# Kernel tuning notes

Hardware: AMD Instinct MI355X
Metric: run time of the kernel (lower is better)

The kernel has to match this reference:

```python
import jax, jax.numpy as jnp
import numpy as np


def setup_inputs() -> dict:
    key = jax.random.key(0)
    ks = jax.random.split(key, 7)
    SEQ, B, IN, H, OUT = 1024, 1024, 57, 128, 18
    return {
        "line_tensor": jax.random.normal(ks[0], (SEQ, B, IN), dtype=jnp.float32),
        "W_ih": jax.random.normal(ks[1], (H, IN), dtype=jnp.float32) * 0.1,
        "b_ih": jax.random.normal(ks[2], (H,), dtype=jnp.float32) * 0.1,
        "W_hh": jax.random.normal(ks[3], (H, H), dtype=jnp.float32) * 0.1,
        "b_hh": jax.random.normal(ks[4], (H,), dtype=jnp.float32) * 0.1,
        "W_ho": jax.random.normal(ks[5], (OUT, H), dtype=jnp.float32) * 0.1,
        "b_ho": jax.random.normal(ks[6], (OUT,), dtype=jnp.float32) * 0.1,
    }


def reference(line_tensor, W_ih, b_ih, W_hh, b_hh, W_ho, b_ho):
    # Elman RNN: h_t = tanh(i2h(x_t) + h2h(h_{t-1})); output = log_softmax(h2o(h_T))
    B = line_tensor.shape[1]
    H = W_hh.shape[0]
    h0 = jnp.zeros((B, H), dtype=line_tensor.dtype)

    def step(h, x):  # x: [B, IN], h: [B, H]
        h = jnp.tanh(x @ W_ih.T + b_ih + h @ W_hh.T + b_hh)
        return h, None

    hT, _ = jax.lax.scan(step, h0, line_tensor)
    logits = hT @ W_ho.T + b_ho  # [B, OUT]
    out = jax.nn.log_softmax(logits, axis=1)
    return (out, hT)
```

## Files before the change

kernel.cpp:

```cpp
#include <hip/hip_runtime.h>
#include <math.h>

#define SEQ   1024
#define BATCH 1024
#define IN_F  57
#define H_F   128
#define OUT_F 18
#define MROWS 16
#define HSTR  136
#define XSTR  72

typedef __attribute__((ext_vector_type(8))) short bf8;
typedef __attribute__((ext_vector_type(4))) float f32x4;

static __device__ __forceinline__ short f2bf(float f) {
    unsigned u = __builtin_bit_cast(unsigned, f);
    u = (u + 0x7FFFu + ((u >> 16) & 1u)) >> 16;
    return (short)u;
}
static __device__ __forceinline__ float bf2f(short s) {
    unsigned u = ((unsigned)(unsigned short)s) << 16;
    return __builtin_bit_cast(float, u);
}

__global__ __launch_bounds__(256) void rnn_mfma_kernel(
    const float* __restrict__ X,
    const float* __restrict__ W_ih,
    const float* __restrict__ b_ih,
    const float* __restrict__ W_hh,
    const float* __restrict__ b_hh,
    const float* __restrict__ W_ho,
    const float* __restrict__ b_ho,
    float* __restrict__ out)
{
    const int tid  = threadIdx.x;
    const int lane = tid & 63;
    const int wv   = tid >> 6;
    const int n16  = lane & 15;
    const int quad = lane >> 4;
    const int b0   = blockIdx.x * MROWS;

    __shared__ short h_lds[2][MROWS][HSTR];
    __shared__ short x_lds[2][MROWS][XSTR];
    __shared__ float logits_lds[MROWS][OUT_F];
    __shared__ float red_lds[MROWS][2];

    const int j0 = wv * 32 + n16;
    const int j1 = j0 + 16;

    const float* wp0 = W_hh + j0 * H_F + quad * 8;
    const float* wp1 = W_hh + j1 * H_F + quad * 8;
#define LDW8(P) ({ \
        f32x4 p_ = *(const f32x4*)(P); \
        f32x4 q_ = *(const f32x4*)((P) + 4); \
        bf8 f_; \
        f_[0]=f2bf(p_[0]); f_[1]=f2bf(p_[1]); f_[2]=f2bf(p_[2]); f_[3]=f2bf(p_[3]); \
        f_[4]=f2bf(q_[0]); f_[5]=f2bf(q_[1]); f_[6]=f2bf(q_[2]); f_[7]=f2bf(q_[3]); \
        f_; })
    bf8 wh00 = LDW8(wp0 +  0), wh01 = LDW8(wp0 + 32), wh02 = LDW8(wp0 + 64), wh03 = LDW8(wp0 + 96);
    bf8 wh10 = LDW8(wp1 +  0), wh11 = LDW8(wp1 + 32), wh12 = LDW8(wp1 + 64), wh13 = LDW8(wp1 + 96);

#define LDWI(J, KS) ({ \
        bf8 f_; \
        _Pragma("unroll") \
        for (int i_ = 0; i_ < 8; ++i_) { \
            int k_ = (KS) * 32 + quad * 8 + i_; \
            f_[i_] = (k_ < IN_F) ? f2bf(W_ih[(J) * IN_F + k_]) : (short)0; \
        } f_; })
    bf8 wi00 = LDWI(j0, 0), wi01 = LDWI(j0, 1), wi10 = LDWI(j1, 0), wi11 = LDWI(j1, 1);

    const float bias0 = b_ih[j0] + b_hh[j0];
    const float bias1 = b_ih[j1] + b_hh[j1];

    const bool  xlane = (tid < 228);
    const size_t tstride = (size_t)BATCH * IN_F;
    const float* xbase = X + (size_t)b0 * IN_F + tid * 4;
    int xm[4], xk[4];
    #pragma unroll
    for (int e = 0; e < 4; ++e) {
        int idx = tid * 4 + e;
        xm[e] = (int)((unsigned)idx / 57u);
        xk[e] = idx - xm[e] * 57;
    }

    for (int i = tid; i < MROWS * HSTR; i += 256) (&h_lds[0][0][0])[i] = 0;
    for (int i = tid; i < 2 * MROWS * XSTR; i += 256) (&x_lds[0][0][0])[i] = 0;
    f32x4 xq0 = {0,0,0,0}, xq1 = {0,0,0,0};
    if (xlane) {
        f32x4 v = *(const f32x4*)(xbase);
        #pragma unroll
        for (int e = 0; e < 4; ++e) x_lds[0][xm[e]][xk[e]] = f2bf(v[e]);
        xq1 = *(const f32x4*)(xbase + 1 * tstride);
        xq0 = *(const f32x4*)(xbase + 2 * tstride);
    }
    __syncthreads();

#define STEP_BARRIER() do { \
        asm volatile("s_waitcnt lgkmcnt(0)" ::: "memory"); \
        __builtin_amdgcn_s_barrier(); \
    } while (0)

#define MFMA __builtin_amdgcn_mfma_f32_16x16x32_bf16
#define STEP(CB, NB, T, XS) do { \
         \
        const short* hc = &h_lds[CB][0][0] + n16 * HSTR + quad * 8; \
        const short* xc = &x_lds[CB][0][0] + n16 * XSTR + quad * 8; \
        bf8 ah0 = *(const bf8*)(hc +  0); \
        bf8 ah1 = *(const bf8*)(hc + 32); \
        bf8 ah2 = *(const bf8*)(hc + 64); \
        bf8 ah3 = *(const bf8*)(hc + 96); \
        bf8 ax0 = *(const bf8*)(xc +  0); \
        bf8 ax1 = *(const bf8*)(xc + 32); \
         \
        if (((T) + 1 < SEQ) && xlane) { \
            _Pragma("unroll") \
            for (int e = 0; e < 4; ++e) x_lds[NB][xm[e]][xk[e]] = f2bf(XS[e]); \
        } \
         \
        if (((T) + 3 < SEQ) && xlane) \
            XS = *(const f32x4*)(xbase + (size_t)((T) + 3) * tstride); \
         \
        f32x4 c0a = {bias0, bias0, bias0, bias0}, c0b = {0.f, 0.f, 0.f, 0.f}; \
        f32x4 c1a = {bias1, bias1, bias1, bias1}, c1b = {0.f, 0.f, 0.f, 0.f}; \
        c0a = MFMA(ah0, wh00, c0a, 0, 0, 0); \
        c1a = MFMA(ah0, wh10, c1a, 0, 0, 0); \
        c0b = MFMA(ah1, wh01, c0b, 0, 0, 0); \
        c1b = MFMA(ah1, wh11, c1b, 0, 0, 0); \
        c0a = MFMA(ah2, wh02, c0a, 0, 0, 0); \
        c1a = MFMA(ah2, wh12, c1a, 0, 0, 0); \
        c0b = MFMA(ah3, wh03, c0b, 0, 0, 0); \
        c1b = MFMA(ah3, wh13, c1b, 0, 0, 0); \
        c0a = MFMA(ax0, wi00, c0a, 0, 0, 0); \
        c1a = MFMA(ax0, wi10, c1a, 0, 0, 0); \
        c0b = MFMA(ax1, wi01, c0b, 0, 0, 0); \
        c1b = MFMA(ax1, wi11, c1b, 0, 0, 0); \
        short* hn = &h_lds[NB][0][0]; \
        _Pragma("unroll") \
        for (int r = 0; r < 4; ++r) { \
            int m = quad * 4 + r; \
            float z0 = fminf(fmaxf(c0a[r] + c0b[r], -9.f), 9.f); \
            float e0 = __expf(2.f * z0); \
            hn[m * HSTR + j0] = f2bf((e0 - 1.f) * __builtin_amdgcn_rcpf(e0 + 1.f)); \
            float z1 = fminf(fmaxf(c1a[r] + c1b[r], -9.f), 9.f); \
            float e1 = __expf(2.f * z1); \
            hn[m * HSTR + j1] = f2bf((e1 - 1.f) * __builtin_amdgcn_rcpf(e1 + 1.f)); \
        } \
        STEP_BARRIER(); \
    } while (0)

    for (int t = 0; t < SEQ; t += 2) {
        STEP(0, 1, t,     xq1);
        STEP(1, 0, t + 1, xq0);
    }
#undef STEP
#undef MFMA

    float* hT = out + (size_t)BATCH * OUT_F;
    #pragma unroll
    for (int r = 0; r < (MROWS * H_F) / 256; ++r) {
        int idx = tid + r * 256;
        int m = idx >> 7, k = idx & 127;
        hT[(size_t)(b0 + m) * H_F + k] = bf2f(h_lds[0][m][k]);
    }

    for (int idx = tid; idx < MROWS * OUT_F; idx += 256) {
        int m = idx / OUT_F, o = idx - m * OUT_F;
        float acc = b_ho[o];
        for (int k = 0; k < H_F; ++k)
            acc = fmaf(bf2f(h_lds[0][m][k]), W_ho[o * H_F + k], acc);
        logits_lds[m][o] = acc;
    }
    __syncthreads();

    if (tid < MROWS) {
        float mx = -1e30f;
        #pragma unroll
        for (int o = 0; o < OUT_F; ++o) mx = fmaxf(mx, logits_lds[tid][o]);
        float s = 0.f;
        #pragma unroll
        for (int o = 0; o < OUT_F; ++o) s += expf(logits_lds[tid][o] - mx);
        red_lds[tid][0] = mx;
        red_lds[tid][1] = logf(s);
    }
    __syncthreads();

    for (int idx = tid; idx < MROWS * OUT_F; idx += 256) {
        int m = idx / OUT_F, o = idx - m * OUT_F;
        out[(size_t)(b0 + m) * OUT_F + o] =
            logits_lds[m][o] - red_lds[m][0] - red_lds[m][1];
    }
}

extern "C" void kernel_launch(void* const* d_in, const int* in_sizes, int n_in,
                              void* d_out, int out_size, void* d_ws, size_t ws_size,
                              hipStream_t stream) {
    const float* X    = (const float*)d_in[0];
    const float* W_ih = (const float*)d_in[1];
    const float* b_ih = (const float*)d_in[2];
    const float* W_hh = (const float*)d_in[3];
    const float* b_hh = (const float*)d_in[4];
    const float* W_ho = (const float*)d_in[5];
    const float* b_ho = (const float*)d_in[6];
    float* out = (float*)d_out;

    rnn_mfma_kernel<<<dim3(BATCH / MROWS), dim3(256), 0, stream>>>(
        X, W_ih, b_ih, W_hh, b_hh, W_ho, b_ho, out);
}
```

Measured before the change: 841.3 us.

## Transpose MFMA operands for packed h stores and use hardware bf16 pack

Swaps the A/B operands of the MFMA so each lane's output holds four consecutive hidden units for one batch row. Each lane can then write h as a single 8-byte packed store instead of eight scalar short stores. The tanh is simplified to 1-2/(e+1) with one clamp, and conversions use v_cvt_pk_bf16_f32. The x staging is remapped to row-aligned 4-float chunks plus a scalar tail, which avoids division-based indexing. The aim is to cut LDS store instructions and ALU work on the serial per-step critical path.

```diff
diff --git a/kernel.cpp b/kernel.cpp
--- a/kernel.cpp
+++ b/kernel.cpp
@@ -12,6 +12,7 @@
 
 typedef __attribute__((ext_vector_type(8))) short bf8;
 typedef __attribute__((ext_vector_type(4))) float f32x4;
+typedef __attribute__((ext_vector_type(2))) unsigned u32x2;
 
 static __device__ __forceinline__ short f2bf(float f) {
     unsigned u = __builtin_bit_cast(unsigned, f);
@@ -21,6 +22,11 @@
 static __device__ __forceinline__ float bf2f(short s) {
     unsigned u = ((unsigned)(unsigned short)s) << 16;
     return __builtin_bit_cast(float, u);
+}
+static __device__ __forceinline__ unsigned pk2bf(float a, float b) {
+    unsigned r;
+    asm("v_cvt_pk_bf16_f32 %0, %1, %2" : "=v"(r) : "v"(a), "v"(b));
+    return r;
 }
 
 __global__ __launch_bounds__(256) void rnn_mfma_kernel(
@@ -69,29 +75,49 @@
         } f_; })
     bf8 wi00 = LDWI(j0, 0), wi01 = LDWI(j0, 1), wi10 = LDWI(j1, 0), wi11 = LDWI(j1, 1);
 
-    const float bias0 = b_ih[j0] + b_hh[j0];
-    const float bias1 = b_ih[j1] + b_hh[j1];
-
-    const bool  xlane = (tid < 228);
+    const int jq0 = wv * 32 + 4 * quad;
+    f32x4 biasA, biasB;
+    {
+        f32x4 a0 = *(const f32x4*)(b_ih + jq0);
+        f32x4 a1 = *(const f32x4*)(b_hh + jq0);
+        biasA = a0 + a1;
+        f32x4 b0v = *(const f32x4*)(b_ih + jq0 + 16);
+        f32x4 b1v = *(const f32x4*)(b_hh + jq0 + 16);
+        biasB = b0v + b1v;
+    }
+
+    const int xs  = tid & 15;
+    const int xm_ = tid >> 4;
+    const int xk0 = xs * 4;
+    const bool xv = (xs < 14);
+    const bool x1 = (xs == 14);
     const size_t tstride = (size_t)BATCH * IN_F;
-    const float* xbase = X + (size_t)b0 * IN_F + tid * 4;
-    int xm[4], xk[4];
-    #pragma unroll
-    for (int e = 0; e < 4; ++e) {
-        int idx = tid * 4 + e;
-        xm[e] = (int)((unsigned)idx / 57u);
-        xk[e] = idx - xm[e] * 57;
-    }
+    const float* xb4 = X + (size_t)(b0 + xm_) * IN_F + xk0;
+    const float* xb1 = X + (size_t)(b0 + xm_) * IN_F + 56;
+
+#define XSTAGE(NB, V, S) do { \
+        if (xv) { \
+            u32x2 w_; \
+            w_[0] = pk2bf((V)[0], (V)[1]); \
+            w_[1] = pk2bf((V)[2], (V)[3]); \
+            *(u32x2*)&x_lds[NB][xm_][xk0] = w_; \
+        } else if (x1) { \
+            x_lds[NB][xm_][56] = f2bf(S); \
+        } } while (0)
 
     for (int i = tid; i < MROWS * HSTR; i += 256) (&h_lds[0][0][0])[i] = 0;
     for (int i = tid; i < 2 * MROWS * XSTR; i += 256) (&x_lds[0][0][0])[i] = 0;
     f32x4 xq0 = {0,0,0,0}, xq1 = {0,0,0,0};
-    if (xlane) {
-        f32x4 v = *(const f32x4*)(xbase);
-        #pragma unroll
-        for (int e = 0; e < 4; ++e) x_lds[0][xm[e]][xk[e]] = f2bf(v[e]);
-        xq1 = *(const f32x4*)(xbase + 1 * tstride);
-        xq0 = *(const f32x4*)(xbase + 2 * tstride);
+    float xq0s = 0.f, xq1s = 0.f;
+    if (xv) {
+        f32x4 v = *(const f32x4*)xb4;
+        XSTAGE(0, v, 0.f);
+        xq1 = *(const f32x4*)(xb4 + 1 * tstride);
+        xq0 = *(const f32x4*)(xb4 + 2 * tstride);
+    } else if (x1) {
+        x_lds[0][xm_][56] = f2bf(*xb1);
+        xq1s = xb1[1 * tstride];
+        xq0s = xb1[2 * tstride];
     }
     __syncthreads();
 
@@ -100,57 +126,72 @@
         __builtin_amdgcn_s_barrier(); \
     } while (0)
 
+#define TH(Z) ({ \
+        float z_ = fminf((Z), 9.f); \
+        float e_ = __expf(2.f * z_); \
+        fmaf(-2.f, __builtin_amdgcn_rcpf(e_ + 1.f), 1.f); })
+
 #define MFMA __builtin_amdgcn_mfma_f32_16x16x32_bf16
-#define STEP(CB, NB, T, XS) do { \
+#define STEP(CB, NB, T, XS, XSS) do { \
          \
         const short* hc = &h_lds[CB][0][0] + n16 * HSTR + quad * 8; \
         const short* xc = &x_lds[CB][0][0] + n16 * XSTR + quad * 8; \
-        bf8 ah0 = *(const bf8*)(hc +  0); \
-        bf8 ah1 = *(const bf8*)(hc + 32); \
-        bf8 ah2 = *(const bf8*)(hc + 64); \
-        bf8 ah3 = *(const bf8*)(hc + 96); \
-        bf8 ax0 = *(const bf8*)(xc +  0); \
-        bf8 ax1 = *(const bf8*)(xc + 32); \
-         \
-        if (((T) + 1 < SEQ) && xlane) { \
-            _Pragma("unroll") \
-            for (int e = 0; e < 4; ++e) x_lds[NB][xm[e]][xk[e]] = f2bf(XS[e]); \
+        bf8 bh0 = *(const bf8*)(hc +  0); \
+        bf8 bh1 = *(const bf8*)(hc + 32); \
+        bf8 bh2 = *(const bf8*)(hc + 64); \
+        bf8 bh3 = *(const bf8*)(hc + 96); \
+        bf8 bx0 = *(const bf8*)(xc +  0); \
+        bf8 bx1 = *(const bf8*)(xc + 32); \
+         \
+        if ((T) + 1 < SEQ) XSTAGE(NB, XS, XSS); \
+         \
+        if ((T) + 3 < SEQ) { \
+            if (xv)      XS  = *(const f32x4*)(xb4 + (size_t)((T) + 3) * tstride); \
+            else if (x1) XSS = xb1[(size_t)((T) + 3) * tstride]; \
         } \
          \
-        if (((T) + 3 < SEQ) && xlane) \
-            XS = *(const f32x4*)(xbase + (size_t)((T) + 3) * tstride); \
-         \
-        f32x4 c0a = {bias0, bias0, bias0, bias0}, c0b = {0.f, 0.f, 0.f, 0.f}; \
-        f32x4 c1a = {bias1, bias1, bias1, bias1}, c1b = {0.f, 0.f, 0.f, 0.f}; \
-        c0a = MFMA(ah0, wh00, c0a, 0, 0, 0); \
-        c1a = MFMA(ah0, wh10, c1a, 0, 0, 0); \
-        c0b = MFMA(ah1, wh01, c0b, 0, 0, 0); \
-        c1b = MFMA(ah1, wh11, c1b, 0, 0, 0); \
-        c0a = MFMA(ah2, wh02, c0a, 0, 0, 0); \
-        c1a = MFMA(ah2, wh12, c1a, 0, 0, 0); \
-        c0b = MFMA(ah3, wh03, c0b, 0, 0, 0); \
-        c1b = MFMA(ah3, wh13, c1b, 0, 0, 0); \
-        c0a = MFMA(ax0, wi00, c0a, 0, 0, 0); \
-        c1a = MFMA(ax0, wi10, c1a, 0, 0, 0); \
-        c0b = MFMA(ax1, wi01, c0b, 0, 0, 0); \
-        c1b = MFMA(ax1, wi11, c1b, 0, 0, 0); \
-        short* hn = &h_lds[NB][0][0]; \
-        _Pragma("unroll") \
-        for (int r = 0; r < 4; ++r) { \
-            int m = quad * 4 + r; \
-            float z0 = fminf(fmaxf(c0a[r] + c0b[r], -9.f), 9.f); \
-            float e0 = __expf(2.f * z0); \
-            hn[m * HSTR + j0] = f2bf((e0 - 1.f) * __builtin_amdgcn_rcpf(e0 + 1.f)); \
-            float z1 = fminf(fmaxf(c1a[r] + c1b[r], -9.f), 9.f); \
-            float e1 = __expf(2.f * z1); \
-            hn[m * HSTR + j1] = f2bf((e1 - 1.f) * __builtin_amdgcn_rcpf(e1 + 1.f)); \
+        f32x4 c0a = biasA, c0b = {0.f, 0.f, 0.f, 0.f}; \
+        f32x4 c1a = biasB, c1b = {0.f, 0.f, 0.f, 0.f}; \
+        c0a = MFMA(wh00, bh0, c0a, 0, 0, 0); \
+        c1a = MFMA(wh10, bh0, c1a, 0, 0, 0); \
+        c0b = MFMA(wh01, bh1, c0b, 0, 0, 0); \
+        c1b = MFMA(wh11, bh1, c1b, 0, 0, 0); \
+        c0a = MFMA(wh02, bh2, c0a, 0, 0, 0); \
+        c1a = MFMA(wh12, bh2, c1a, 0, 0, 0); \
+        c0b = MFMA(wh03, bh3, c0b, 0, 0, 0); \
+        c1b = MFMA(wh13, bh3, c1b, 0, 0, 0); \
+        c0a = MFMA(wi00, bx0, c0a, 0, 0, 0); \
+        c1a = MFMA(wi10, bx0, c1a, 0, 0, 0); \
+        c0b = MFMA(wi01, bx1, c0b, 0, 0, 0); \
+        c1b = MFMA(wi11, bx1, c1b, 0, 0, 0); \
+         \
+         \
+        { \
+            float t0_ = TH(c0a[0] + c0b[0]); \
+            float t1_ = TH(c0a[1] + c0b[1]); \
+            float t2_ = TH(c0a[2] + c0b[2]); \
+            float t3_ = TH(c0a[3] + c0b[3]); \
+            u32x2 w_; \
+            w_[0] = pk2bf(t0_, t1_); \
+            w_[1] = pk2bf(t2_, t3_); \
+            *(u32x2*)&h_lds[NB][n16][jq0] = w_; \
+        } \
+        { \
+            float t0_ = TH(c1a[0] + c1b[0]); \
+            float t1_ = TH(c1a[1] + c1b[1]); \
+            float t2_ = TH(c1a[2] + c1b[2]); \
+            float t3_ = TH(c1a[3] + c1b[3]); \
+            u32x2 w_; \
+            w_[0] = pk2bf(t0_, t1_); \
+            w_[1] = pk2bf(t2_, t3_); \
+            *(u32x2*)&h_lds[NB][n16][jq0 + 16] = w_; \
         } \
         STEP_BARRIER(); \
     } while (0)
 
     for (int t = 0; t < SEQ; t += 2) {
-        STEP(0, 1, t,     xq1);
-        STEP(1, 0, t + 1, xq0);
+        STEP(0, 1, t,     xq1, xq1s);
+        STEP(1, 0, t + 1, xq0, xq0s);
     }
 #undef STEP
 #undef MFMA
```

Result: slower. 1.231 ms (+46.3%).

## Split hidden columns across eight waves, one 16-column tile each

Applied to the files above, without the earlier changes.

The block grows from 256 to 512 threads, so each of eight waves computes a single 16-column output tile instead of two. The per-step MFMA chain and tanh work per wave are halved, which shortens the serial critical path of each recurrence step. The cost is a barrier across twice as many waves every timestep and more waves per CU, with only 64 blocks in the grid. The x-loading lanes (tid<228) are unchanged.

```diff
diff --git a/kernel.cpp b/kernel.cpp
--- a/kernel.cpp
+++ b/kernel.cpp
@@ -9,6 +9,7 @@
 #define MROWS 16
 #define HSTR  136
 #define XSTR  72
+#define NT    512
 
 typedef __attribute__((ext_vector_type(8))) short bf8;
 typedef __attribute__((ext_vector_type(4))) float f32x4;
@@ -23,7 +24,7 @@
     return __builtin_bit_cast(float, u);
 }
 
-__global__ __launch_bounds__(256) void rnn_mfma_kernel(
+__global__ __launch_bounds__(NT) void rnn_mfma_kernel(
     const float* __restrict__ X,
     const float* __restrict__ W_ih,
     const float* __restrict__ b_ih,
@@ -45,11 +46,9 @@
     __shared__ float logits_lds[MROWS][OUT_F];
     __shared__ float red_lds[MROWS][2];
 
-    const int j0 = wv * 32 + n16;
-    const int j1 = j0 + 16;
+    const int j0 = wv * 16 + n16;
 
     const float* wp0 = W_hh + j0 * H_F + quad * 8;
-    const float* wp1 = W_hh + j1 * H_F + quad * 8;
 #define LDW8(P) ({ \
         f32x4 p_ = *(const f32x4*)(P); \
         f32x4 q_ = *(const f32x4*)((P) + 4); \
@@ -57,8 +56,7 @@
         f_[0]=f2bf(p_[0]); f_[1]=f2bf(p_[1]); f_[2]=f2bf(p_[2]); f_[3]=f2bf(p_[3]); \
         f_[4]=f2bf(q_[0]); f_[5]=f2bf(q_[1]); f_[6]=f2bf(q_[2]); f_[7]=f2bf(q_[3]); \
         f_; })
-    bf8 wh00 = LDW8(wp0 +  0), wh01 = LDW8(wp0 + 32), wh02 = LDW8(wp0 + 64), wh03 = LDW8(wp0 + 96);
-    bf8 wh10 = LDW8(wp1 +  0), wh11 = LDW8(wp1 + 32), wh12 = LDW8(wp1 + 64), wh13 = LDW8(wp1 + 96);
+    bf8 wh0 = LDW8(wp0 +  0), wh1 = LDW8(wp0 + 32), wh2 = LDW8(wp0 + 64), wh3 = LDW8(wp0 + 96);
 
 #define LDWI(J, KS) ({ \
         bf8 f_; \
@@ -67,10 +65,9 @@
             int k_ = (KS) * 32 + quad * 8 + i_; \
             f_[i_] = (k_ < IN_F) ? f2bf(W_ih[(J) * IN_F + k_]) : (short)0; \
         } f_; })
-    bf8 wi00 = LDWI(j0, 0), wi01 = LDWI(j0, 1), wi10 = LDWI(j1, 0), wi11 = LDWI(j1, 1);
+    bf8 wi0 = LDWI(j0, 0), wi1 = LDWI(j0, 1);
 
     const float bias0 = b_ih[j0] + b_hh[j0];
-    const float bias1 = b_ih[j1] + b_hh[j1];
 
     const bool  xlane = (tid < 228);
     const size_t tstride = (size_t)BATCH * IN_F;
@@ -83,8 +80,8 @@
         xk[e] = idx - xm[e] * 57;
     }
 
-    for (int i = tid; i < MROWS * HSTR; i += 256) (&h_lds[0][0][0])[i] = 0;
-    for (int i = tid; i < 2 * MROWS * XSTR; i += 256) (&x_lds[0][0][0])[i] = 0;
+    for (int i = tid; i < MROWS * HSTR; i += NT) (&h_lds[0][0][0])[i] = 0;
+    for (int i = tid; i < 2 * MROWS * XSTR; i += NT) (&x_lds[0][0][0])[i] = 0;
     f32x4 xq0 = {0,0,0,0}, xq1 = {0,0,0,0};
     if (xlane) {
         f32x4 v = *(const f32x4*)(xbase);
@@ -120,30 +117,20 @@
         if (((T) + 3 < SEQ) && xlane) \
             XS = *(const f32x4*)(xbase + (size_t)((T) + 3) * tstride); \
          \
-        f32x4 c0a = {bias0, bias0, bias0, bias0}, c0b = {0.f, 0.f, 0.f, 0.f}; \
-        f32x4 c1a = {bias1, bias1, bias1, bias1}, c1b = {0.f, 0.f, 0.f, 0.f}; \
-        c0a = MFMA(ah0, wh00, c0a, 0, 0, 0); \
-        c1a = MFMA(ah0, wh10, c1a, 0, 0, 0); \
-        c0b = MFMA(ah1, wh01, c0b, 0, 0, 0); \
-        c1b = MFMA(ah1, wh11, c1b, 0, 0, 0); \
-        c0a = MFMA(ah2, wh02, c0a, 0, 0, 0); \
-        c1a = MFMA(ah2, wh12, c1a, 0, 0, 0); \
-        c0b = MFMA(ah3, wh03, c0b, 0, 0, 0); \
-        c1b = MFMA(ah3, wh13, c1b, 0, 0, 0); \
-        c0a = MFMA(ax0, wi00, c0a, 0, 0, 0); \
-        c1a = MFMA(ax0, wi10, c1a, 0, 0, 0); \
-        c0b = MFMA(ax1, wi01, c0b, 0, 0, 0); \
-        c1b = MFMA(ax1, wi11, c1b, 0, 0, 0); \
+        f32x4 ca = {bias0, bias0, bias0, bias0}, cb = {0.f, 0.f, 0.f, 0.f}; \
+        ca = MFMA(ah0, wh0, ca, 0, 0, 0); \
+        cb = MFMA(ah1, wh1, cb, 0, 0, 0); \
+        ca = MFMA(ah2, wh2, ca, 0, 0, 0); \
+        cb = MFMA(ah3, wh3, cb, 0, 0, 0); \
+        ca = MFMA(ax0, wi0, ca, 0, 0, 0); \
+        cb = MFMA(ax1, wi1, cb, 0, 0, 0); \
         short* hn = &h_lds[NB][0][0]; \
         _Pragma("unroll") \
         for (int r = 0; r < 4; ++r) { \
             int m = quad * 4 + r; \
-            float z0 = fminf(fmaxf(c0a[r] + c0b[r], -9.f), 9.f); \
-            float e0 = __expf(2.f * z0); \
-            hn[m * HSTR + j0] = f2bf((e0 - 1.f) * __builtin_amdgcn_rcpf(e0 + 1.f)); \
-            float z1 = fminf(fmaxf(c1a[r] + c1b[r], -9.f), 9.f); \
-            float e1 = __expf(2.f * z1); \
-            hn[m * HSTR + j1] = f2bf((e1 - 1.f) * __builtin_amdgcn_rcpf(e1 + 1.f)); \
+            float z = fminf(fmaxf(ca[r] + cb[r], -9.f), 9.f); \
+            float e = __expf(2.f * z); \
+            hn[m * HSTR + j0] = f2bf((e - 1.f) * __builtin_amdgcn_rcpf(e + 1.f)); \
         } \
         STEP_BARRIER(); \
     } while (0)
@@ -157,13 +144,13 @@
 
     float* hT = out + (size_t)BATCH * OUT_F;
     #pragma unroll
-    for (int r = 0; r < (MROWS * H_F) / 256; ++r) {
-        int idx = tid + r * 256;
+    for (int r = 0; r < (MROWS * H_F) / NT; ++r) {
+        int idx = tid + r * NT;
         int m = idx >> 7, k = idx & 127;
         hT[(size_t)(b0 + m) * H_F + k] = bf2f(h_lds[0][m][k]);
     }
 
-    for (int idx = tid; idx < MROWS * OUT_F; idx += 256) {
+    for (int idx = tid; idx < MROWS * OUT_F; idx += NT) {
         int m = idx / OUT_F, o = idx - m * OUT_F;
         float acc = b_ho[o];
         for (int k = 0; k < H_F; ++k)
@@ -184,7 +171,7 @@
     }
     __syncthreads();
 
-    for (int idx = tid; idx < MROWS * OUT_F; idx += 256) {
+    for (int idx = tid; idx < MROWS * OUT_F; idx += NT) {
         int m = idx / OUT_F, o = idx - m * OUT_F;
         out[(size_t)(b0 + m) * OUT_F + o] =
             logits_lds[m][o] - red_lds[m][0] - red_lds[m][1];
@@ -203,6 +190,6 @@
     const float* b_ho = (const float*)d_in[6];
     float* out = (float*)d_out;
 
-    rnn_mfma_kernel<<<dim3(BATCH / MROWS), dim3(256), 0, stream>>>(
+    rnn_mfma_kernel<<<dim3(BATCH / MROWS), dim3(NT), 0, stream>>>(
         X, W_ih, b_ih, W_hh, b_hh, W_ho, b_ho, out);
 }
```

Result: faster. 809.2 us (-3.8%).
